# Performance work log

Measured on AMD Instinct MI355X. Metric: run time of the kernel, lower is better.

## Reference

```python
import jax, jax.numpy as jnp
import numpy as np

N, E = 20000, 5000
IN_FT, OUT_FT = 128, 128
DENSITY = 0.01  # fraction of nonzeros in the incidence matrix


def setup_inputs() -> dict:
    key = jax.random.key(0)
    kx, kh, kw, kb = jax.random.split(key, 4)
    X = jax.random.normal(kx, (N, IN_FT), dtype=jnp.float32)
    H = (jax.random.uniform(kh, (N, E)) < DENSITY).astype(jnp.float32)
    # xavier_normal_ with gain=0.01
    xav_std = 0.01 * np.sqrt(2.0 / (IN_FT + OUT_FT))
    weight_trans = jax.random.normal(kw, (IN_FT, OUT_FT), dtype=jnp.float32) * xav_std
    bias = jax.random.normal(kb, (OUT_FT,), dtype=jnp.float32) * 0.01
    return {"X": X, "H": H, "weight_trans": weight_trans, "bias": bias}


def reference(X, H, weight_trans, bias):
    # X: [N, in_ft], H: [N, E] incidence
    Xw = X @ weight_trans                      # [N, out_ft]
    DV = jnp.sum(H, axis=1) + 1e-12            # node degrees, [N]
    DE = jnp.sum(H, axis=0) + 1e-12            # hyperedge degrees, [E]
    # G = diag(1/DV) @ H @ diag(1/DE) @ H^T applied to Xw, computed in the
    # efficient order without materializing the NxN matrix G:
    M = H.T @ Xw                               # [E, out_ft]
    M = M / DE[:, None]                        # diag(1/DE) scaling
    out = H @ M                                # [N, out_ft]
    out = out / DV[:, None]                    # diag(1/DV) scaling
    out = out + bias
    return jax.nn.relu(out)
```

## Files before the change

kernel.cpp:

```cpp
#include <hip/hip_runtime.h>
#include <hip/hip_bf16.h>

typedef unsigned long long u64;

#define N_NODES 20000
#define N_EDGES 5000
#define FT 128
#define NT 20
#define NRG 313
#define ROW_U64 80
#define COL_STRIDE 5120
#define MAX_DEG 320
#define MAX_NDEG 128

__global__ __launch_bounds__(256) void x_to_bf16(
    const float2* __restrict__ X2, __hip_bfloat162* __restrict__ Xb2) {
  int i = blockIdx.x * 256 + threadIdx.x;
  Xb2[i] = __float22bfloat162_rn(X2[i]);
}

__global__ __launch_bounds__(256) void scan_rows(
    const float4* __restrict__ H4, u64* __restrict__ Hbt) {
  const int wid = threadIdx.x >> 6, lane = threadIdx.x & 63;
  const int gw = blockIdx.x * 4 + wid;
  const int r0 = gw * 4;
  u64 mlo = 0, mhi = 0;
  float4 A[10], B[10];

  {
    const float4* rp = H4 + (size_t)r0 * 1250;
#pragma unroll
    for (int q = 0; q < 10; ++q) A[q] = rp[q * 64 + lane];
  }
  for (int rr = 0; rr < 4; ++rr) {
    const float4* rp = H4 + (size_t)(r0 + rr) * 1250;
#pragma unroll
    for (int q = 0; q < 9; ++q) B[q] = rp[(10 + q) * 64 + lane];
    B[9] = make_float4(0.f, 0.f, 0.f, 0.f);
    if (lane < 34) B[9] = rp[19 * 64 + lane];
#pragma unroll
    for (int q = 0; q < 10; ++q) {
      u64 b0 = __ballot(A[q].x != 0.f);
      u64 b1 = __ballot(A[q].y != 0.f);
      u64 b2 = __ballot(A[q].z != 0.f);
      u64 b3 = __ballot(A[q].w != 0.f);
      int vp = 4 * q;
      mlo = (lane == vp)     ? b0 : mlo;
      mlo = (lane == vp + 1) ? b1 : mlo;
      mlo = (lane == vp + 2) ? b2 : mlo;
      mlo = (lane == vp + 3) ? b3 : mlo;
    }
    if (rr < 3) {
      const float4* rn = H4 + (size_t)(r0 + rr + 1) * 1250;
#pragma unroll
      for (int q = 0; q < 10; ++q) A[q] = rn[q * 64 + lane];
    }
#pragma unroll
    for (int q = 0; q < 10; ++q) {
      u64 b0 = __ballot(B[q].x != 0.f);
      u64 b1 = __ballot(B[q].y != 0.f);
      u64 b2 = __ballot(B[q].z != 0.f);
      u64 b3 = __ballot(B[q].w != 0.f);
      const int g = 10 + q;
      if (g < 16) {
        const int vp = 4 * g;
        mlo = (lane == vp)     ? b0 : mlo;
        mlo = (lane == vp + 1) ? b1 : mlo;
        mlo = (lane == vp + 2) ? b2 : mlo;
        mlo = (lane == vp + 3) ? b3 : mlo;
      } else {
        const int vp = 4 * g - 64;
        mhi = (lane == vp)     ? b0 : mhi;
        mhi = (lane == vp + 1) ? b1 : mhi;
        mhi = (lane == vp + 2) ? b2 : mhi;
        mhi = (lane == vp + 3) ? b3 : mhi;
      }
    }
    u64* hp = Hbt + (size_t)(r0 + rr) * ROW_U64;
    hp[lane] = mlo;
    if (lane < 16) hp[64 + lane] = mhi;
    mlo = 0; mhi = 0;
  }
}

__global__ __launch_bounds__(256) void transpose_bm(
    const u64* __restrict__ Hbt, u64* __restrict__ HbtT) {
  const int wid = threadIdx.x >> 6, lane = threadIdx.x & 63;
  const int gw = blockIdx.x * 4 + wid;
  const int t = gw % NT, rg = gw / NT;
  const int r = rg * 64 + lane;
  u64 w0 = 0, w1 = 0, w2 = 0, w3 = 0;
  if (r < N_NODES) {
    const u64* hp = Hbt + (size_t)r * ROW_U64 + t * 4;
    w0 = hp[0]; w1 = hp[1]; w2 = hp[2]; w3 = hp[3];
  }
  u64 t0 = 0, t1 = 0, t2 = 0, t3 = 0;
  for (int l = 0; l < 64; ++l) {
    u64 c0 = __ballot((w0 >> l) & 1ull);
    u64 c1 = __ballot((w1 >> l) & 1ull);
    u64 c2 = __ballot((w2 >> l) & 1ull);
    u64 c3 = __ballot((w3 >> l) & 1ull);
    const bool keep = (lane == l);
    t0 = keep ? c0 : t0;  t1 = keep ? c1 : t1;
    t2 = keep ? c2 : t2;  t3 = keep ? c3 : t3;
  }
  u64* op = HbtT + (size_t)rg * COL_STRIDE + t * 256 + 4 * lane;
  op[0] = t0; op[1] = t1; op[2] = t2; op[3] = t3;
}

__global__ __launch_bounds__(256) void edge_gather(
    const __hip_bfloat162* __restrict__ Xb2,
    const u64* __restrict__ HbtT,
    float2* __restrict__ P2, int* __restrict__ de) {
  __shared__ int sidx[4][MAX_DEG];
  const int wid = threadIdx.x >> 6, lane = threadIdx.x & 63;
  const int e = blockIdx.x * 4 + wid;

  u64 cm[5];
#pragma unroll
  for (int q = 0; q < 5; ++q) {
    int u = q * 64 + lane;
    cm[q] = (u < NRG) ? HbtT[(size_t)u * COL_STRIDE + e] : 0ull;
  }
  int cnt = 0;
#pragma unroll
  for (int q = 0; q < 5; ++q) cnt += __popcll(cm[q]);
  int off = cnt;
  for (int d = 1; d < 64; d <<= 1) {
    int v = __shfl_up(off, d);
    if (lane >= d) off += v;
  }
  int total = __shfl(off, 63);
  off -= cnt;
#pragma unroll
  for (int q = 0; q < 5; ++q) {
    u64 w = cm[q];
    int rbase = q * 4096 + lane * 64;
    while (w) {
      int b = __ffsll(w) - 1;
      w &= w - 1;
      if (off < MAX_DEG) sidx[wid][off] = rbase + b;
      ++off;
    }
  }
  __builtin_amdgcn_s_waitcnt(0);
  int tt = min(total, MAX_DEG);

  float sx = 0.f, sy = 0.f;
  int g = 0;
  for (; g + 16 <= tt; g += 16) {
    int nn[16];
#pragma unroll
    for (int q = 0; q < 16; ++q) nn[q] = sidx[wid][g + q];
    float2 aa[16];
#pragma unroll
    for (int q = 0; q < 16; ++q) aa[q] = __bfloat1622float2(Xb2[nn[q] * 64 + lane]);
#pragma unroll
    for (int q = 0; q < 16; ++q) { sx += aa[q].x; sy += aa[q].y; }
  }
  for (; g < tt; ++g) {
    float2 a2 = __bfloat1622float2(Xb2[sidx[wid][g] * 64 + lane]);
    sx += a2.x; sy += a2.y;
  }
  P2[e * 64 + lane] = make_float2(sx, sy);
  if (lane == 0) de[e] = total;
}

__global__ __launch_bounds__(256) void gemm_M(
    const float* __restrict__ P, const float* __restrict__ W,
    const int* __restrict__ de, float* __restrict__ M) {
  int f = threadIdx.x & (FT - 1);
  int half = threadIdx.x >> 7;
  int base = blockIdx.x * 16 + half * 8;
#pragma unroll
  for (int g = 0; g < 8; g += 4) {
    int e = base + g;
    if (e >= N_EDGES) break;
    const float* p0 = P + (e + 0) * FT;
    const float* p1 = P + (e + 1) * FT;
    const float* p2 = P + (e + 2) * FT;
    const float* p3 = P + (e + 3) * FT;
    float a0 = 0.f, a1 = 0.f, a2 = 0.f, a3 = 0.f;
#pragma unroll 4
    for (int k = 0; k < FT; ++k) {
      float w = W[k * FT + f];
      a0 += p0[k] * w; a1 += p1[k] * w; a2 += p2[k] * w; a3 += p3[k] * w;
    }
    M[(e + 0) * FT + f] = a0 / ((float)de[e + 0] + 1e-12f);
    M[(e + 1) * FT + f] = a1 / ((float)de[e + 1] + 1e-12f);
    M[(e + 2) * FT + f] = a2 / ((float)de[e + 2] + 1e-12f);
    M[(e + 3) * FT + f] = a3 / ((float)de[e + 3] + 1e-12f);
  }
}

__global__ __launch_bounds__(256) void row_apply(
    const u64* __restrict__ Hbt,
    const float2* __restrict__ M2, const float2* __restrict__ bias2,
    float2* __restrict__ out2) {
  __shared__ int eidx[4][MAX_NDEG];
  const int wid = threadIdx.x >> 6, lane = threadIdx.x & 63;
  const int n = blockIdx.x * 4 + wid;
  const u64* hp = Hbt + (size_t)n * ROW_U64;
  u64 mlo = hp[lane];
  u64 mhi = (lane < ROW_U64 - 64) ? hp[64 + lane] : 0ull;
  int cnt = __popcll(mlo) + __popcll(mhi);
  int off = cnt;
  for (int d = 1; d < 64; d <<= 1) {
    int v = __shfl_up(off, d);
    if (lane >= d) off += v;
  }
  int total = __shfl(off, 63);
  off -= cnt;
  {
    int eb = (lane >> 2) * 256 + (lane & 3);
    u64 w = mlo;
    while (w) {
      int b = __ffsll(w) - 1; w &= w - 1;
      if (off < MAX_NDEG) eidx[wid][off] = eb + 4 * b;
      ++off;
    }
    int vp = 64 + lane;
    eb = (vp >> 2) * 256 + (vp & 3);
    w = mhi;
    while (w) {
      int b = __ffsll(w) - 1; w &= w - 1;
      if (off < MAX_NDEG) eidx[wid][off] = eb + 4 * b;
      ++off;
    }
  }
  __builtin_amdgcn_s_waitcnt(0);
  int tt = min(total, MAX_NDEG);

  float sx = 0.f, sy = 0.f;
  int g = 0;
  for (; g + 8 <= tt; g += 8) {
    int ee[8];
#pragma unroll
    for (int q = 0; q < 8; ++q) ee[q] = eidx[wid][g + q];
    float2 vv[8];
#pragma unroll
    for (int q = 0; q < 8; ++q) vv[q] = M2[(size_t)ee[q] * 64 + lane];
#pragma unroll
    for (int q = 0; q < 8; ++q) { sx += vv[q].x; sy += vv[q].y; }
  }
  for (; g < tt; ++g) {
    float2 v = M2[(size_t)eidx[wid][g] * 64 + lane];
    sx += v.x; sy += v.y;
  }
  float inv = 1.f / ((float)total + 1e-12f);
  float2 bb = bias2[lane];
  float2 o;
  o.x = fmaxf(fmaf(sx, inv, bb.x), 0.f);
  o.y = fmaxf(fmaf(sy, inv, bb.y), 0.f);
  out2[(size_t)n * 64 + lane] = o;
}

extern "C" void kernel_launch(void* const* d_in, const int* in_sizes, int n_in,
                              void* d_out, int out_size, void* d_ws, size_t ws_size,
                              hipStream_t stream) {
  const float* X    = (const float*)d_in[0];
  const float* H    = (const float*)d_in[1];
  const float* W    = (const float*)d_in[2];
  const float* bias = (const float*)d_in[3];
  float* out = (float*)d_out;

  int* ws = (int*)d_ws;
  u64* Hbt             = (u64*)ws;
  u64* HbtT            = (u64*)(ws + 3200000);
  __hip_bfloat162* Xb2 = (__hip_bfloat162*)(ws + 6476800);
  float* P             = (float*)(ws + 7756800);
  int* de              = ws + 8396800;
  float* M             = (float*)(ws + 8401920);

  x_to_bf16   <<<5000, 256, 0, stream>>>((const float2*)X, Xb2);
  scan_rows   <<<1250, 256, 0, stream>>>((const float4*)H, Hbt);
  transpose_bm<<<1565, 256, 0, stream>>>(Hbt, HbtT);
  edge_gather <<<1250, 256, 0, stream>>>(Xb2, HbtT, (float2*)P, de);
  gemm_M      <<<313, 256, 0, stream>>>(P, W, de, M);
  row_apply   <<<5000, 256, 0, stream>>>(Hbt, (const float2*)M,
                                         (const float2*)bias, (float2*)out);
}
```

Measured before the change: 651.2 us.

## Stream H rows through LDS with async global_load_lds double buffering

Replaces the register-staged row scan of the dense incidence matrix with a kernel that DMAs each row chunk straight into LDS via global_load_lds, double-buffered per wavefront with explicit vmcnt waits. Each wave now processes 2 rows instead of 4, launched over twice as many blocks. The aim is to cut register pressure and keep more memory requests in flight on the 400MB H read, which dominates runtime. The hand-tuned waitcnt values and LDS reuse ordering are fragile: a wrong count could race on the buffers.

```diff
diff --git a/kernel.cpp b/kernel.cpp
--- a/kernel.cpp
+++ b/kernel.cpp
@@ -13,74 +13,87 @@
 #define MAX_DEG 320
 #define MAX_NDEG 128
 
+#define GLOBAL_TO_LDS(g, l) __builtin_amdgcn_global_load_lds(                  \
+    (const __attribute__((address_space(1))) void*)(g),                        \
+    (__attribute__((address_space(3))) void*)(l), 16, 0, 0)
+#define WAITVM(n) __builtin_amdgcn_s_waitcnt(0x0F70 | (n))
+
 __global__ __launch_bounds__(256) void x_to_bf16(
     const float2* __restrict__ X2, __hip_bfloat162* __restrict__ Xb2) {
   int i = blockIdx.x * 256 + threadIdx.x;
   Xb2[i] = __float22bfloat162_rn(X2[i]);
 }
 
-__global__ __launch_bounds__(256) void scan_rows(
-    const float4* __restrict__ H4, u64* __restrict__ Hbt) {
-  const int wid = threadIdx.x >> 6, lane = threadIdx.x & 63;
-  const int gw = blockIdx.x * 4 + wid;
-  const int r0 = gw * 4;
+__global__ __launch_bounds__(256) void scan_dma(
+    const float* __restrict__ H, u64* __restrict__ Hbt) {
+  __shared__ float lds[4][2][1024];
+  const int wid = threadIdx.x >> 6, lane = threadIdx.x & 63;
+  const int r0 = (blockIdx.x * 4 + wid) * 2;
+  float* const lb0 = lds[wid][0];
+  float* const lb1 = lds[wid][1];
+
   u64 mlo = 0, mhi = 0;
-  float4 A[10], B[10];
-
-  {
-    const float4* rp = H4 + (size_t)r0 * 1250;
-#pragma unroll
-    for (int q = 0; q < 10; ++q) A[q] = rp[q * 64 + lane];
-  }
-  for (int rr = 0; rr < 4; ++rr) {
-    const float4* rp = H4 + (size_t)(r0 + rr) * 1250;
-#pragma unroll
-    for (int q = 0; q < 9; ++q) B[q] = rp[(10 + q) * 64 + lane];
-    B[9] = make_float4(0.f, 0.f, 0.f, 0.f);
-    if (lane < 34) B[9] = rp[19 * 64 + lane];
-#pragma unroll
-    for (int q = 0; q < 10; ++q) {
-      u64 b0 = __ballot(A[q].x != 0.f);
-      u64 b1 = __ballot(A[q].y != 0.f);
-      u64 b2 = __ballot(A[q].z != 0.f);
-      u64 b3 = __ballot(A[q].w != 0.f);
-      int vp = 4 * q;
-      mlo = (lane == vp)     ? b0 : mlo;
-      mlo = (lane == vp + 1) ? b1 : mlo;
-      mlo = (lane == vp + 2) ? b2 : mlo;
-      mlo = (lane == vp + 3) ? b3 : mlo;
-    }
-    if (rr < 3) {
-      const float4* rn = H4 + (size_t)(r0 + rr + 1) * 1250;
-#pragma unroll
-      for (int q = 0; q < 10; ++q) A[q] = rn[q * 64 + lane];
-    }
-#pragma unroll
-    for (int q = 0; q < 10; ++q) {
-      u64 b0 = __ballot(B[q].x != 0.f);
-      u64 b1 = __ballot(B[q].y != 0.f);
-      u64 b2 = __ballot(B[q].z != 0.f);
-      u64 b3 = __ballot(B[q].w != 0.f);
-      const int g = 10 + q;
-      if (g < 16) {
-        const int vp = 4 * g;
-        mlo = (lane == vp)     ? b0 : mlo;
-        mlo = (lane == vp + 1) ? b1 : mlo;
-        mlo = (lane == vp + 2) ? b2 : mlo;
-        mlo = (lane == vp + 3) ? b3 : mlo;
-      } else {
-        const int vp = 4 * g - 64;
-        mhi = (lane == vp)     ? b0 : mhi;
-        mhi = (lane == vp + 1) ? b1 : mhi;
-        mhi = (lane == vp + 2) ? b2 : mhi;
-        mhi = (lane == vp + 3) ? b3 : mhi;
+
+#define ISSUE(t) do {                                                          \
+    const int s_ = (t) % 5;                                                    \
+    const float* rp_ = H + (size_t)(r0 + (t) / 5) * 5000 + s_ * 1024;          \
+    float* l_ = ((t) & 1) ? lb1 : lb0;                                         \
+    _Pragma("unroll")                                                          \
+    for (int c_ = 0; c_ < 4; ++c_) {                                           \
+      if (s_ * 4 + c_ < 19) {                                                  \
+        GLOBAL_TO_LDS(rp_ + c_ * 256 + lane * 4, l_ + c_ * 256);               \
+      } else {                                                                 \
+        if (lane >= 34)        \
+          *(float4*)(l_ + c_ * 256 + lane * 4) = make_float4(0.f,0.f,0.f,0.f); \
+        if (lane < 34)                \
+          GLOBAL_TO_LDS(rp_ + c_ * 256 + lane * 4, l_ + c_ * 256);             \
+      }                                                                        \
+    }                                                                          \
+  } while (0)
+
+  ISSUE(0);
+#pragma unroll
+  for (int t = 0; t < 10; ++t) {
+    if (t + 1 < 10) ISSUE(t + 1);
+    if (t == 9)      WAITVM(0);
+    else if (t == 5) WAITVM(6);
+    else             WAITVM(4);
+    __builtin_amdgcn_sched_barrier(0);
+    {
+      float* l_ = (t & 1) ? lb1 : lb0;
+      const int s_ = t % 5;
+#pragma unroll
+      for (int c = 0; c < 4; ++c) {
+        float4 v = *(float4*)(l_ + c * 256 + lane * 4);
+        u64 b0 = __ballot(v.x != 0.f);
+        u64 b1 = __ballot(v.y != 0.f);
+        u64 b2 = __ballot(v.z != 0.f);
+        u64 b3 = __ballot(v.w != 0.f);
+        const int g = s_ * 4 + c;
+        if (g < 16) {
+          const int vp = 4 * g;
+          mlo = (lane == vp)     ? b0 : mlo;
+          mlo = (lane == vp + 1) ? b1 : mlo;
+          mlo = (lane == vp + 2) ? b2 : mlo;
+          mlo = (lane == vp + 3) ? b3 : mlo;
+        } else {
+          const int vp = 4 * g - 64;
+          mhi = (lane == vp)     ? b0 : mhi;
+          mhi = (lane == vp + 1) ? b1 : mhi;
+          mhi = (lane == vp + 2) ? b2 : mhi;
+          mhi = (lane == vp + 3) ? b3 : mhi;
+        }
       }
-    }
-    u64* hp = Hbt + (size_t)(r0 + rr) * ROW_U64;
-    hp[lane] = mlo;
-    if (lane < 16) hp[64 + lane] = mhi;
-    mlo = 0; mhi = 0;
-  }
+      if (t % 5 == 4) {
+        u64* hp = Hbt + (size_t)(r0 + t / 5) * ROW_U64;
+        hp[lane] = mlo;
+        if (lane < 16) hp[64 + lane] = mhi;
+        mlo = 0; mhi = 0;
+      }
+    }
+    __builtin_amdgcn_sched_barrier(0);
+  }
+#undef ISSUE
 }
 
 __global__ __launch_bounds__(256) void transpose_bm(
@@ -273,7 +286,7 @@
   float* M             = (float*)(ws + 8401920);
 
   x_to_bf16   <<<5000, 256, 0, stream>>>((const float2*)X, Xb2);
-  scan_rows   <<<1250, 256, 0, stream>>>((const float4*)H, Hbt);
+  scan_dma    <<<2500, 256, 0, stream>>>(H, Hbt);
   transpose_bm<<<1565, 256, 0, stream>>>(Hbt, HbtT);
   edge_gather <<<1250, 256, 0, stream>>>(Xb2, HbtT, (float2*)P, de);
   gemm_M      <<<313, 256, 0, stream>>>(P, W, de, M);
```

New measurement: 655.1 us. Within noise of the previous version (+0.6%).
